# Kernel tuning notes

Hardware: AMD Instinct MI355X
Metric: run time of the kernel (lower is better)

Reference implementation:

```python
import jax, jax.numpy as jnp
import numpy as np

B, S, E, H = 2, 2048, 1024, 16
DH = E // H


def setup_inputs() -> dict:
    key = jax.random.key(0)
    ks = jax.random.split(key, 7)
    sc = 1.0 / np.sqrt(E)
    return {
        "x": jax.random.normal(ks[0], (B, S, E), dtype=jnp.float32),
        "Wq": jax.random.uniform(ks[1], (E, E), jnp.float32, -sc, sc),
        "bq": jax.random.uniform(ks[2], (E,), jnp.float32, -sc, sc),
        "Wk": jax.random.uniform(ks[3], (E, E), jnp.float32, -sc, sc),
        "bk": jax.random.uniform(ks[4], (E,), jnp.float32, -sc, sc),
        "Wv": jax.random.uniform(ks[5], (E, E), jnp.float32, -sc, sc),
        "bv": jax.random.uniform(ks[6], (E,), jnp.float32, -sc, sc),
    }


def reference(x, Wq, bq, Wk, bk, Wv, bv):
    b, s, _ = x.shape
    # torch Linear: y = x @ W.T + b
    q = (x @ Wq.T + bq).reshape(b, s, H, DH).transpose(0, 2, 1, 3)  # [B,H,S,Dh]
    k = (x @ Wk.T + bk).reshape(b, s, H, DH).transpose(0, 2, 1, 3)
    v = (x @ Wv.T + bv).reshape(b, s, H, DH).transpose(0, 2, 1, 3)
    # original einsum labels treat axis1 as 's' and axis2 as 'h'/'v':
    # scores: [B, S_q, H, S_k]  (softmax over keys, last axis)
    scores = jnp.einsum('bshd,bsvd->bhsv', q, k) / np.sqrt(DH)
    probs = jax.nn.softmax(scores, axis=-1)
    # out: [B, H, S, Dh] per original label permutation
    out = jnp.einsum('bhsv,bsvd->bshd', probs, v)
    # original reshapes WITHOUT transposing heads back (faithful quirk)
    return out.reshape(b, s, E)
```

## Files before the change

kernel.cpp:

```cpp
#include <hip/hip_runtime.h>
#include <hip/hip_bf16.h>

#define Bb 2
#define Ss 2048
#define Ee 1024
#define Hh 16
#define Dh 64
#define QSCALE 0.18033688011112042f

using u16 = unsigned short;
using u32 = unsigned int;
typedef __attribute__((ext_vector_type(8))) short short8;
typedef __attribute__((ext_vector_type(8))) u16 ushort8;
typedef __attribute__((ext_vector_type(4))) float f32x4;
typedef __attribute__((ext_vector_type(16))) float f32x16;
typedef __attribute__((ext_vector_type(4))) u32 uint4v;

#define GAS __attribute__((address_space(1)))
#define LAS __attribute__((address_space(3)))

__device__ __forceinline__ void gload16(const u16* g, u16* l) {
  __builtin_amdgcn_global_load_lds((const GAS unsigned int*)g,
                                   (LAS unsigned int*)l, 16, 0, 0);
}

__device__ __forceinline__ u16 f2bf(float f) {
  union { float f; unsigned u; } v;
  v.f = f;
  unsigned u = v.u;
  unsigned r = (u + 0x7FFFu + ((u >> 16) & 1u)) >> 16;
  return (u16)r;
}

__global__ __launch_bounds__(256) void cvt_all(
    const float* __restrict__ x, const float* __restrict__ wq,
    const float* __restrict__ wk, const float* __restrict__ wv,
    u16* __restrict__ xo, u16* __restrict__ wqo, u16* __restrict__ wko,
    u16* __restrict__ wvo) {
  const int b = blockIdx.x;
  const float* s;
  u16* d;
  int i;
  if (b < 2048) {
    s = x; d = xo; i = b * 256 + threadIdx.x;
  } else {
    const int wb = b - 2048;
    const int which = wb >> 9;
    s = which == 0 ? wq : (which == 1 ? wk : wv);
    d = which == 0 ? wqo : (which == 1 ? wko : wvo);
    i = (wb & 511) * 256 + threadIdx.x;
  }
  const float* p = s + (size_t)i * 8;
  ushort8 o;
#pragma unroll
  for (int j = 0; j < 8; ++j) o[j] = f2bf(p[j]);
  *(ushort8*)(d + (size_t)i * 8) = o;
}

__global__ __launch_bounds__(512, 2) void qkv_gemm(
    const u16* __restrict__ Xb, const u16* __restrict__ Wcat,
    const float* __restrict__ bq, const float* __restrict__ bk,
    const float* __restrict__ bv,
    u16* __restrict__ Qo, u16* __restrict__ Ko, u16* __restrict__ Vo) {
  __shared__ u16 Ast[2][128][32];
  __shared__ u16 Bst[2][384][32];
  const int tid = threadIdx.x;
  const int lane = tid & 63;
  const int w = tid >> 6;
  const int wm = w >> 2, wn = w & 3;
  const int c = lane & 15, g = lane >> 4;
  const int flat = blockIdx.x;
  const int m0 = (flat >> 3) * 128;
  const int n0 = (flat & 7) * 384;

  bool isv[6];
#pragma unroll
  for (int nf = 0; nf < 6; ++nf) isv[nf] = (n0 + wn * 96 + nf * 16) >= 2048;

  f32x4 acc[4][6] = {};

  {
    const int elemA = tid * 8;
    gload16(Xb + (size_t)(m0 + (elemA >> 5)) * 1024 + (elemA & 31),
            &Ast[0][0][0] + w * 512);
#pragma unroll
    for (int i = 0; i < 3; ++i) {
      const int elem = i * 4096 + tid * 8;
      gload16(Wcat + (size_t)(n0 + (elem >> 5)) * 1024 + (elem & 31),
              &Bst[0][0][0] + i * 4096 + w * 512);
    }
  }
  __syncthreads();

  for (int kt = 0; kt < 32; ++kt) {
    if (kt < 31) {
      const int k0n = (kt + 1) * 32;
      const int nb = (kt + 1) & 1;
      const int elemA = tid * 8;
      gload16(Xb + (size_t)(m0 + (elemA >> 5)) * 1024 + k0n + (elemA & 31),
              &Ast[nb][0][0] + w * 512);
#pragma unroll
      for (int i = 0; i < 3; ++i) {
        const int elem = i * 4096 + tid * 8;
        gload16(Wcat + (size_t)(n0 + (elem >> 5)) * 1024 + k0n + (elem & 31),
                &Bst[nb][0][0] + i * 4096 + w * 512);
      }
    }
    const int cb = kt & 1;
    short8 af[4], bf[6];
#pragma unroll
    for (int mf = 0; mf < 4; ++mf)
      af[mf] = *(const short8*)&Ast[cb][wm * 64 + mf * 16 + c][g * 8];
#pragma unroll
    for (int nf = 0; nf < 6; ++nf)
      bf[nf] = *(const short8*)&Bst[cb][wn * 96 + nf * 16 + c][g * 8];
#pragma unroll
    for (int nf = 0; nf < 6; ++nf) {
      if (isv[nf]) {
#pragma unroll
        for (int mf = 0; mf < 4; ++mf)
          acc[mf][nf] = __builtin_amdgcn_mfma_f32_16x16x32_bf16(
              bf[nf], af[mf], acc[mf][nf], 0, 0, 0);
      } else {
#pragma unroll
        for (int mf = 0; mf < 4; ++mf)
          acc[mf][nf] = __builtin_amdgcn_mfma_f32_16x16x32_bf16(
              af[mf], bf[nf], acc[mf][nf], 0, 0, 0);
      }
    }
    __syncthreads();
  }

#pragma unroll
  for (int nf = 0; nf < 6; ++nf) {
    const int nc0 = n0 + wn * 96 + nf * 16;
    if (nc0 < 2048) {
      const int which = nc0 >> 10;
      u16* Oo = which == 0 ? Qo : Ko;
      const float* bias = which == 0 ? bq : bk;
      const float scl = which == 0 ? QSCALE : 1.0f;
      const int ncol = (nc0 & 1023) + c;
      const float bval = bias[ncol];
      const int hh = ncol >> 6, dd = ncol & 63;
#pragma unroll
      for (int mf = 0; mf < 4; ++mf) {
#pragma unroll
        for (int r = 0; r < 4; ++r) {
          const int m = m0 + wm * 64 + mf * 16 + g * 4 + r;
          const int bb = m >> 11, ss = m & 2047;
          Oo[(((size_t)bb * Hh + hh) * Ss + ss) * Dh + dd] =
              f2bf((acc[mf][nf][r] + bval) * scl);
        }
      }
    } else {
#pragma unroll
      for (int r = 0; r < 4; ++r) {
        const int ncol = (nc0 - 2048) + g * 4 + r;
        const float bval = bv[ncol];
        const int hh = ncol >> 6, dd = ncol & 63;
#pragma unroll
        for (int mf = 0; mf < 4; ++mf) {
          const int m = m0 + wm * 64 + mf * 16 + c;
          const int bb = m >> 11, ss = m & 2047;
          Vo[(((size_t)bb * Hh + hh) * Dh + dd) * Ss + ss] =
              f2bf(acc[mf][nf][r] + bval);
        }
      }
    }
  }
}

__global__ __launch_bounds__(256, 2) void attn(
    const u16* __restrict__ Q, const u16* __restrict__ K,
    const u16* __restrict__ VT, float* __restrict__ out) {
  __shared__ u16 Kst[2][2][64][64];
  __shared__ u16 Vst[2][2][64][64];
  const int tid = threadIdx.x;
  const int lane = tid & 63;
  const int w = tid >> 6;
  const int c5 = lane & 31, g2 = lane >> 5;
  const int flat = blockIdx.x;
  const int bh = (flat & 7) * 4 + ((flat >> 3) >> 4);
  const int q0 = ((flat >> 3) & 15) * 128;
  const u16* Qb = Q + (size_t)bh * Ss * Dh;
  const u16* Kb = K + (size_t)bh * Ss * Dh;
  const u16* VTb = VT + (size_t)bh * Ss * Dh;

  const int srow = lane >> 3;
  const int scolx = ((lane & 7) * 8) ^ (srow * 8);

  const u16* Qrow = Qb + (size_t)(q0 + w * 32 + c5) * Dh + 8 * g2;
  short8 qf[4];
#pragma unroll
  for (int s = 0; s < 4; ++s) qf[s] = *(const short8*)(Qrow + 16 * s);

  short8 ones;
#pragma unroll
  for (int j = 0; j < 8; ++j) ones[j] = (short)0x3F80;
  f32x16 ZZ = {};

  const int cxor = (c5 & 7) << 4;
  int slot[4];
#pragma unroll
  for (int s = 0; s < 4; ++s) slot[s] = c5 * 128 + ((32 * s + 16 * g2) ^ cxor);

#pragma unroll
  for (int sub = 0; sub < 2; ++sub) {
#pragma unroll
    for (int p = 0; p < 2; ++p) {
      const int row = w * 8 + srow + p * 32;
      gload16(Kb + (size_t)(sub * 64 + row) * Dh + scolx,
              &Kst[0][sub][0][0] + w * 512 + p * 2048);
      gload16(VTb + (size_t)row * Ss + sub * 64 + scolx,
              &Vst[0][sub][0][0] + w * 512 + p * 2048);
    }
  }

  f32x16 oacc0 = {}, oacc1 = {}, lacc = {};

  for (int kt = 0; kt < 16; ++kt) {
    __syncthreads();
    if (kt < 15) {
      const int k0n = (kt + 1) * 128;
      const int nb = (kt + 1) & 1;
#pragma unroll
      for (int sub = 0; sub < 2; ++sub) {
#pragma unroll
        for (int p = 0; p < 2; ++p) {
          const int row = w * 8 + srow + p * 32;
          gload16(Kb + (size_t)(k0n + sub * 64 + row) * Dh + scolx,
                  &Kst[nb][sub][0][0] + w * 512 + p * 2048);
          gload16(VTb + (size_t)row * Ss + k0n + sub * 64 + scolx,
                  &Vst[nb][sub][0][0] + w * 512 + p * 2048);
        }
      }
    }
    const char* kb0 = (const char*)&Kst[kt & 1][0][0][0];
    const char* kb1 = (const char*)&Kst[kt & 1][1][0][0];
    const char* vb0 = (const char*)&Vst[kt & 1][0][0][0];
    const char* vb1 = (const char*)&Vst[kt & 1][1][0][0];

    f32x16 sA0, sA1, sB0, sB1;
    __builtin_amdgcn_s_setprio(1);
    {
      short8 ka0 = *(const short8*)(kb0 + slot[0]);
      short8 ka1 = *(const short8*)(kb0 + slot[0] + 4096);
      short8 kc0 = *(const short8*)(kb1 + slot[0]);
      short8 kc1 = *(const short8*)(kb1 + slot[0] + 4096);
      sA0 = __builtin_amdgcn_mfma_f32_32x32x16_bf16(ka0, qf[0], ZZ, 0, 0, 0);
      sA1 = __builtin_amdgcn_mfma_f32_32x32x16_bf16(ka1, qf[0], ZZ, 0, 0, 0);
      sB0 = __builtin_amdgcn_mfma_f32_32x32x16_bf16(kc0, qf[0], ZZ, 0, 0, 0);
      sB1 = __builtin_amdgcn_mfma_f32_32x32x16_bf16(kc1, qf[0], ZZ, 0, 0, 0);
    }
#pragma unroll
    for (int s = 1; s < 4; ++s) {
      short8 ka0 = *(const short8*)(kb0 + slot[s]);
      short8 ka1 = *(const short8*)(kb0 + slot[s] + 4096);
      short8 kc0 = *(const short8*)(kb1 + slot[s]);
      short8 kc1 = *(const short8*)(kb1 + slot[s] + 4096);
      sA0 = __builtin_amdgcn_mfma_f32_32x32x16_bf16(ka0, qf[s], sA0, 0, 0, 0);
      sA1 = __builtin_amdgcn_mfma_f32_32x32x16_bf16(ka1, qf[s], sA1, 0, 0, 0);
      sB0 = __builtin_amdgcn_mfma_f32_32x32x16_bf16(kc0, qf[s], sB0, 0, 0, 0);
      sB1 = __builtin_amdgcn_mfma_f32_32x32x16_bf16(kc1, qf[s], sB1, 0, 0, 0);
    }
    __builtin_amdgcn_s_setprio(0);

    u32 pkvA[2][8];
#pragma unroll
    for (int i = 0; i < 8; ++i) {
      const u32 e0 = __builtin_bit_cast(u32, __builtin_amdgcn_exp2f(sA0[2 * i]));
      const u32 e1 = __builtin_bit_cast(u32, __builtin_amdgcn_exp2f(sA0[2 * i + 1]));
      pkvA[0][i] = __builtin_amdgcn_perm(e1, e0, 0x07060302u);
    }
#pragma unroll
    for (int i = 0; i < 8; ++i) {
      const u32 e0 = __builtin_bit_cast(u32, __builtin_amdgcn_exp2f(sA1[2 * i]));
      const u32 e1 = __builtin_bit_cast(u32, __builtin_amdgcn_exp2f(sA1[2 * i + 1]));
      pkvA[1][i] = __builtin_amdgcn_perm(e1, e0, 0x07060302u);
    }

    __builtin_amdgcn_s_setprio(1);
#pragma unroll
    for (int sp = 0; sp < 4; ++sp) {
      const int kb = sp >> 1, sg = sp & 1;
      u32 x0 = pkvA[kb][4 * sg + 0], y0 = pkvA[kb][4 * sg + 2];
      u32 x1 = pkvA[kb][4 * sg + 1], y1 = pkvA[kb][4 * sg + 3];
      asm("v_permlane32_swap_b32 %0, %1" : "+v"(x0), "+v"(y0));
      asm("v_permlane32_swap_b32 %0, %1" : "+v"(x1), "+v"(y1));
      uint4v av;
      av[0] = x0; av[1] = x1; av[2] = y0; av[3] = y1;
      const short8 af = __builtin_bit_cast(short8, av);
      short8 vf0 = *(const short8*)(vb0 + slot[sp]);
      short8 vf1 = *(const short8*)(vb0 + slot[sp] + 4096);
      lacc = __builtin_amdgcn_mfma_f32_32x32x16_bf16(af, ones, lacc, 0, 0, 0);
      oacc0 = __builtin_amdgcn_mfma_f32_32x32x16_bf16(af, vf0, oacc0, 0, 0, 0);
      oacc1 = __builtin_amdgcn_mfma_f32_32x32x16_bf16(af, vf1, oacc1, 0, 0, 0);
    }
    __builtin_amdgcn_s_setprio(0);

    u32 pkvB[2][8];
#pragma unroll
    for (int i = 0; i < 8; ++i) {
      const u32 e0 = __builtin_bit_cast(u32, __builtin_amdgcn_exp2f(sB0[2 * i]));
      const u32 e1 = __builtin_bit_cast(u32, __builtin_amdgcn_exp2f(sB0[2 * i + 1]));
      pkvB[0][i] = __builtin_amdgcn_perm(e1, e0, 0x07060302u);
    }
#pragma unroll
    for (int i = 0; i < 8; ++i) {
      const u32 e0 = __builtin_bit_cast(u32, __builtin_amdgcn_exp2f(sB1[2 * i]));
      const u32 e1 = __builtin_bit_cast(u32, __builtin_amdgcn_exp2f(sB1[2 * i + 1]));
      pkvB[1][i] = __builtin_amdgcn_perm(e1, e0, 0x07060302u);
    }

    __builtin_amdgcn_s_setprio(1);
#pragma unroll
    for (int sp = 0; sp < 4; ++sp) {
      const int kb = sp >> 1, sg = sp & 1;
      u32 x0 = pkvB[kb][4 * sg + 0], y0 = pkvB[kb][4 * sg + 2];
      u32 x1 = pkvB[kb][4 * sg + 1], y1 = pkvB[kb][4 * sg + 3];
      asm("v_permlane32_swap_b32 %0, %1" : "+v"(x0), "+v"(y0));
      asm("v_permlane32_swap_b32 %0, %1" : "+v"(x1), "+v"(y1));
      uint4v av;
      av[0] = x0; av[1] = x1; av[2] = y0; av[3] = y1;
      const short8 af = __builtin_bit_cast(short8, av);
      short8 vf0 = *(const short8*)(vb1 + slot[sp]);
      short8 vf1 = *(const short8*)(vb1 + slot[sp] + 4096);
      lacc = __builtin_amdgcn_mfma_f32_32x32x16_bf16(af, ones, lacc, 0, 0, 0);
      oacc0 = __builtin_amdgcn_mfma_f32_32x32x16_bf16(af, vf0, oacc0, 0, 0, 0);
      oacc1 = __builtin_amdgcn_mfma_f32_32x32x16_bf16(af, vf1, oacc1, 0, 0, 0);
    }
    __builtin_amdgcn_s_setprio(0);
  }

  float* ob = out + (size_t)bh * Ss * Dh;
#pragma unroll
  for (int r = 0; r < 16; ++r) {
    const float inv = 1.0f / lacc[r];
    const int q = q0 + w * 32 + (r & 3) + 8 * (r >> 2) + 4 * g2;
    ob[(size_t)q * Dh + c5] = oacc0[r] * inv;
    ob[(size_t)q * Dh + 32 + c5] = oacc1[r] * inv;
  }
}

extern "C" void kernel_launch(void* const* d_in, const int* in_sizes, int n_in,
                              void* d_out, int out_size, void* d_ws, size_t ws_size,
                              hipStream_t stream) {
  const float* x = (const float*)d_in[0];
  const float* Wq = (const float*)d_in[1];
  const float* bq = (const float*)d_in[2];
  const float* Wk = (const float*)d_in[3];
  const float* bk = (const float*)d_in[4];
  const float* Wv = (const float*)d_in[5];
  const float* bv = (const float*)d_in[6];
  float* out = (float*)d_out;

  if (ws_size < (size_t)(38u << 20)) return;
  char* ws = (char*)d_ws;
  u16* Qb = (u16*)(ws + (size_t)(0u << 20));
  u16* Kb = (u16*)(ws + (size_t)(8u << 20));
  u16* Vb = (u16*)(ws + (size_t)(16u << 20));
  u16* Xb = (u16*)(ws + (size_t)(24u << 20));
  u16* Wqb = (u16*)(ws + (size_t)(32u << 20));
  u16* Wkb = (u16*)(ws + (size_t)(34u << 20));
  u16* Wvb = (u16*)(ws + (size_t)(36u << 20));

  cvt_all<<<3584, 256, 0, stream>>>(x, Wq, Wk, Wv, Xb, Wqb, Wkb, Wvb);
  qkv_gemm<<<256, 512, 0, stream>>>(Xb, Wqb, bq, bk, bv, Qb, Kb, Vb);
  attn<<<512, 256, 0, stream>>>(Qb, Kb, Vb, out);
}
```

Baseline: 99.38 us.

## Split attention key range across two wave groups with LDS reduction

The attention kernel now launches 512 threads per block. Two groups of four waves each process half of the key sequence (1024 keys) for the same 128 queries, using 64-key tiles per iteration instead of 128. Partial output accumulators and row sums are combined through shared memory before the final normalisation and store. This doubles the waves in flight per block to hide latency, at the cost of extra barriers, a shared-memory reduction and half the work per iteration.

```diff
diff --git a/kernel.cpp b/kernel.cpp
--- a/kernel.cpp
+++ b/kernel.cpp
@@ -170,26 +170,29 @@
   }
 }
 
-__global__ __launch_bounds__(256, 2) void attn(
+__global__ __launch_bounds__(512, 4) void attn(
     const u16* __restrict__ Q, const u16* __restrict__ K,
     const u16* __restrict__ VT, float* __restrict__ out) {
-  __shared__ u16 Kst[2][2][64][64];
-  __shared__ u16 Vst[2][2][64][64];
+  __shared__ __align__(16) u16 Kst[2][2][64][64];
+  __shared__ __align__(16) u16 Vst[2][2][64][64];
   const int tid = threadIdx.x;
   const int lane = tid & 63;
   const int w = tid >> 6;
+  const int wq = w & 3;
+  const int half = w >> 2;
   const int c5 = lane & 31, g2 = lane >> 5;
   const int flat = blockIdx.x;
   const int bh = (flat & 7) * 4 + ((flat >> 3) >> 4);
   const int q0 = ((flat >> 3) & 15) * 128;
   const u16* Qb = Q + (size_t)bh * Ss * Dh;
-  const u16* Kb = K + (size_t)bh * Ss * Dh;
+  const int kcol0 = half * 1024;
+  const u16* Kb = K + (size_t)bh * Ss * Dh + (size_t)kcol0 * Dh;
   const u16* VTb = VT + (size_t)bh * Ss * Dh;
 
   const int srow = lane >> 3;
   const int scolx = ((lane & 7) * 8) ^ (srow * 8);
 
-  const u16* Qrow = Qb + (size_t)(q0 + w * 32 + c5) * Dh + 8 * g2;
+  const u16* Qrow = Qb + (size_t)(q0 + wq * 32 + c5) * Dh + 8 * g2;
   short8 qf[4];
 #pragma unroll
   for (int s = 0; s < 4; ++s) qf[s] = *(const short8*)(Qrow + 16 * s);
@@ -204,16 +207,14 @@
 #pragma unroll
   for (int s = 0; s < 4; ++s) slot[s] = c5 * 128 + ((32 * s + 16 * g2) ^ cxor);
 
-#pragma unroll
-  for (int sub = 0; sub < 2; ++sub) {
-#pragma unroll
-    for (int p = 0; p < 2; ++p) {
-      const int row = w * 8 + srow + p * 32;
-      gload16(Kb + (size_t)(sub * 64 + row) * Dh + scolx,
-              &Kst[0][sub][0][0] + w * 512 + p * 2048);
-      gload16(VTb + (size_t)row * Ss + sub * 64 + scolx,
-              &Vst[0][sub][0][0] + w * 512 + p * 2048);
-    }
+  u16* kst_h = &Kst[half][0][0][0];
+  u16* vst_h = &Vst[half][0][0][0];
+
+#pragma unroll
+  for (int p = 0; p < 2; ++p) {
+    const int row = wq * 8 + srow + p * 32;
+    gload16(Kb + (size_t)row * Dh + scolx, kst_h + wq * 512 + p * 2048);
+    gload16(VTb + (size_t)row * Ss + kcol0 + scolx, vst_h + wq * 512 + p * 2048);
   }
 
   f32x16 oacc0 = {}, oacc1 = {}, lacc = {};
@@ -221,124 +222,109 @@
   for (int kt = 0; kt < 16; ++kt) {
     __syncthreads();
     if (kt < 15) {
-      const int k0n = (kt + 1) * 128;
+      const int k0n = (kt + 1) * 64;
       const int nb = (kt + 1) & 1;
 #pragma unroll
-      for (int sub = 0; sub < 2; ++sub) {
-#pragma unroll
-        for (int p = 0; p < 2; ++p) {
-          const int row = w * 8 + srow + p * 32;
-          gload16(Kb + (size_t)(k0n + sub * 64 + row) * Dh + scolx,
-                  &Kst[nb][sub][0][0] + w * 512 + p * 2048);
-          gload16(VTb + (size_t)row * Ss + k0n + sub * 64 + scolx,
-                  &Vst[nb][sub][0][0] + w * 512 + p * 2048);
-        }
-      }
-    }
-    const char* kb0 = (const char*)&Kst[kt & 1][0][0][0];
-    const char* kb1 = (const char*)&Kst[kt & 1][1][0][0];
-    const char* vb0 = (const char*)&Vst[kt & 1][0][0][0];
-    const char* vb1 = (const char*)&Vst[kt & 1][1][0][0];
-
-    f32x16 sA0, sA1, sB0, sB1;
+      for (int p = 0; p < 2; ++p) {
+        const int row = wq * 8 + srow + p * 32;
+        gload16(Kb + (size_t)(k0n + row) * Dh + scolx,
+                kst_h + nb * 4096 + wq * 512 + p * 2048);
+        gload16(VTb + (size_t)row * Ss + kcol0 + k0n + scolx,
+                vst_h + nb * 4096 + wq * 512 + p * 2048);
+      }
+    }
+    const char* kbuf = (const char*)(kst_h + (kt & 1) * 4096);
+    const char* vbuf = (const char*)(vst_h + (kt & 1) * 4096);
+
+    f32x16 sc0, sc1;
     __builtin_amdgcn_s_setprio(1);
     {
-      short8 ka0 = *(const short8*)(kb0 + slot[0]);
-      short8 ka1 = *(const short8*)(kb0 + slot[0] + 4096);
-      short8 kc0 = *(const short8*)(kb1 + slot[0]);
-      short8 kc1 = *(const short8*)(kb1 + slot[0] + 4096);
-      sA0 = __builtin_amdgcn_mfma_f32_32x32x16_bf16(ka0, qf[0], ZZ, 0, 0, 0);
-      sA1 = __builtin_amdgcn_mfma_f32_32x32x16_bf16(ka1, qf[0], ZZ, 0, 0, 0);
-      sB0 = __builtin_amdgcn_mfma_f32_32x32x16_bf16(kc0, qf[0], ZZ, 0, 0, 0);
-      sB1 = __builtin_amdgcn_mfma_f32_32x32x16_bf16(kc1, qf[0], ZZ, 0, 0, 0);
+      short8 kf0 = *(const short8*)(kbuf + slot[0]);
+      short8 kf1 = *(const short8*)(kbuf + slot[0] + 4096);
+      sc0 = __builtin_amdgcn_mfma_f32_32x32x16_bf16(kf0, qf[0], ZZ, 0, 0, 0);
+      sc1 = __builtin_amdgcn_mfma_f32_32x32x16_bf16(kf1, qf[0], ZZ, 0, 0, 0);
     }
 #pragma unroll
     for (int s = 1; s < 4; ++s) {
-      short8 ka0 = *(const short8*)(kb0 + slot[s]);
-      short8 ka1 = *(const short8*)(kb0 + slot[s] + 4096);
-      short8 kc0 = *(const short8*)(kb1 + slot[s]);
-      short8 kc1 = *(const short8*)(kb1 + slot[s] + 4096);
-      sA0 = __builtin_amdgcn_mfma_f32_32x32x16_bf16(ka0, qf[s], sA0, 0, 0, 0);
-      sA1 = __builtin_amdgcn_mfma_f32_32x32x16_bf16(ka1, qf[s], sA1, 0, 0, 0);
-      sB0 = __builtin_amdgcn_mfma_f32_32x32x16_bf16(kc0, qf[s], sB0, 0, 0, 0);
-      sB1 = __builtin_amdgcn_mfma_f32_32x32x16_bf16(kc1, qf[s], sB1, 0, 0, 0);
+      short8 kf0 = *(const short8*)(kbuf + slot[s]);
+      short8 kf1 = *(const short8*)(kbuf + slot[s] + 4096);
+      sc0 = __builtin_amdgcn_mfma_f32_32x32x16_bf16(kf0, qf[s], sc0, 0, 0, 0);
+      sc1 = __builtin_amdgcn_mfma_f32_32x32x16_bf16(kf1, qf[s], sc1, 0, 0, 0);
     }
     __builtin_amdgcn_s_setprio(0);
 
-    u32 pkvA[2][8];
+    u32 pkv[2][8];
 #pragma unroll
     for (int i = 0; i < 8; ++i) {
-      const u32 e0 = __builtin_bit_cast(u32, __builtin_amdgcn_exp2f(sA0[2 * i]));
-      const u32 e1 = __builtin_bit_cast(u32, __builtin_amdgcn_exp2f(sA0[2 * i + 1]));
-      pkvA[0][i] = __builtin_amdgcn_perm(e1, e0, 0x07060302u);
+      const u32 e0 = __builtin_bit_cast(u32, __builtin_amdgcn_exp2f(sc0[2 * i]));
+      const u32 e1 = __builtin_bit_cast(u32, __builtin_amdgcn_exp2f(sc0[2 * i + 1]));
+      pkv[0][i] = __builtin_amdgcn_perm(e1, e0, 0x07060302u);
     }
 #pragma unroll
     for (int i = 0; i < 8; ++i) {
-      const u32 e0 = __builtin_bit_cast(u32, __builtin_amdgcn_exp2f(sA1[2 * i]));
-      const u32 e1 = __builtin_bit_cast(u32, __builtin_amdgcn_exp2f(sA1[2 * i + 1]));
-      pkvA[1][i] = __builtin_amdgcn_perm(e1, e0, 0x07060302u);
+      const u32 e0 = __builtin_bit_cast(u32, __builtin_amdgcn_exp2f(sc1[2 * i]));
+      const u32 e1 = __builtin_bit_cast(u32, __builtin_amdgcn_exp2f(sc1[2 * i + 1]));
+      pkv[1][i] = __builtin_amdgcn_perm(e1, e0, 0x07060302u);
     }
 
     __builtin_amdgcn_s_setprio(1);
 #pragma unroll
     for (int sp = 0; sp < 4; ++sp) {
       const int kb = sp >> 1, sg = sp & 1;
-      u32 x0 = pkvA[kb][4 * sg + 0], y0 = pkvA[kb][4 * sg + 2];
-      u32 x1 = pkvA[kb][4 * sg + 1], y1 = pkvA[kb][4 * sg + 3];
+      u32 x0 = pkv[kb][4 * sg + 0], y0 = pkv[kb][4 * sg + 2];
+      u32 x1 = pkv[kb][4 * sg + 1], y1 = pkv[kb][4 * sg + 3];
       asm("v_permlane32_swap_b32 %0, %1" : "+v"(x0), "+v"(y0));
       asm("v_permlane32_swap_b32 %0, %1" : "+v"(x1), "+v"(y1));
       uint4v av;
       av[0] = x0; av[1] = x1; av[2] = y0; av[3] = y1;
       const short8 af = __builtin_bit_cast(short8, av);
-      short8 vf0 = *(const short8*)(vb0 + slot[sp]);
-      short8 vf1 = *(const short8*)(vb0 + slot[sp] + 4096);
+      short8 vf0 = *(const short8*)(vbuf + slot[sp]);
+      short8 vf1 = *(const short8*)(vbuf + slot[sp] + 4096);
       lacc = __builtin_amdgcn_mfma_f32_32x32x16_bf16(af, ones, lacc, 0, 0, 0);
       oacc0 = __builtin_amdgcn_mfma_f32_32x32x16_bf16(af, vf0, oacc0, 0, 0, 0);
       oacc1 = __builtin_amdgcn_mfma_f32_32x32x16_bf16(af, vf1, oacc1, 0, 0, 0);
     }
     __builtin_amdgcn_s_setprio(0);
-
-    u32 pkvB[2][8];
-#pragma unroll
-    for (int i = 0; i < 8; ++i) {
-      const u32 e0 = __builtin_bit_cast(u32, __builtin_amdgcn_exp2f(sB0[2 * i]));
-      const u32 e1 = __builtin_bit_cast(u32, __builtin_amdgcn_exp2f(sB0[2 * i + 1]));
-      pkvB[0][i] = __builtin_amdgcn_perm(e1, e0, 0x07060302u);
-    }
-#pragma unroll
-    for (int i = 0; i < 8; ++i) {
-      const u32 e0 = __builtin_bit_cast(u32, __builtin_amdgcn_exp2f(sB1[2 * i]));
-      const u32 e1 = __builtin_bit_cast(u32, __builtin_amdgcn_exp2f(sB1[2 * i + 1]));
-      pkvB[1][i] = __builtin_amdgcn_perm(e1, e0, 0x07060302u);
-    }
-
-    __builtin_amdgcn_s_setprio(1);
-#pragma unroll
-    for (int sp = 0; sp < 4; ++sp) {
-      const int kb = sp >> 1, sg = sp & 1;
-      u32 x0 = pkvB[kb][4 * sg + 0], y0 = pkvB[kb][4 * sg + 2];
-      u32 x1 = pkvB[kb][4 * sg + 1], y1 = pkvB[kb][4 * sg + 3];
-      asm("v_permlane32_swap_b32 %0, %1" : "+v"(x0), "+v"(y0));
-      asm("v_permlane32_swap_b32 %0, %1" : "+v"(x1), "+v"(y1));
-      uint4v av;
-      av[0] = x0; av[1] = x1; av[2] = y0; av[3] = y1;
-      const short8 af = __builtin_bit_cast(short8, av);
-      short8 vf0 = *(const short8*)(vb1 + slot[sp]);
-      short8 vf1 = *(const short8*)(vb1 + slot[sp] + 4096);
-      lacc = __builtin_amdgcn_mfma_f32_32x32x16_bf16(af, ones, lacc, 0, 0, 0);
-      oacc0 = __builtin_amdgcn_mfma_f32_32x32x16_bf16(af, vf0, oacc0, 0, 0, 0);
-      oacc1 = __builtin_amdgcn_mfma_f32_32x32x16_bf16(af, vf1, oacc1, 0, 0, 0);
-    }
-    __builtin_amdgcn_s_setprio(0);
-  }
-
-  float* ob = out + (size_t)bh * Ss * Dh;
-#pragma unroll
-  for (int r = 0; r < 16; ++r) {
-    const float inv = 1.0f / lacc[r];
-    const int q = q0 + w * 32 + (r & 3) + 8 * (r >> 2) + 4 * g2;
-    ob[(size_t)q * Dh + c5] = oacc0[r] * inv;
-    ob[(size_t)q * Dh + 32 + c5] = oacc1[r] * inv;
+  }
+
+  float* sh = (float*)&Kst[0][0][0][0];
+  const int mi = wq * 64 + lane;
+  __syncthreads();
+  if (half) {
+#pragma unroll
+    for (int r = 0; r < 16; ++r) sh[r * 256 + mi] = oacc0[r];
+  }
+  __syncthreads();
+  if (!half) {
+#pragma unroll
+    for (int r = 0; r < 16; ++r) oacc0[r] += sh[r * 256 + mi];
+  }
+  __syncthreads();
+  if (half) {
+#pragma unroll
+    for (int r = 0; r < 16; ++r) sh[r * 256 + mi] = oacc1[r];
+  }
+  __syncthreads();
+  if (!half) {
+#pragma unroll
+    for (int r = 0; r < 16; ++r) oacc1[r] += sh[r * 256 + mi];
+  }
+  __syncthreads();
+  if (half) {
+#pragma unroll
+    for (int r = 0; r < 16; ++r) sh[r * 256 + mi] = lacc[r];
+  }
+  __syncthreads();
+  if (!half) {
+    float* ob = out + (size_t)bh * Ss * Dh;
+#pragma unroll
+    for (int r = 0; r < 16; ++r) {
+      const float lfull = lacc[r] + sh[r * 256 + mi];
+      const float inv = 1.0f / lfull;
+      const int q = q0 + wq * 32 + (r & 3) + 8 * (r >> 2) + 4 * g2;
+      ob[(size_t)q * Dh + c5] = oacc0[r] * inv;
+      ob[(size_t)q * Dh + 32 + c5] = oacc1[r] * inv;
+    }
   }
 }
 
@@ -366,5 +352,5 @@
 
   cvt_all<<<3584, 256, 0, stream>>>(x, Wq, Wk, Wv, Xb, Wqb, Wkb, Wvb);
   qkv_gemm<<<256, 512, 0, stream>>>(Xb, Wqb, bq, bk, bv, Qb, Kb, Vb);
-  attn<<<512, 256, 0, stream>>>(Qb, Kb, Vb, out);
-}
+  attn<<<512, 512, 0, stream>>>(Qb, Kb, Vb, out);
+}
```

Result: no change. 100.4 us (+1.0%).
